# Kernel optimization log

Hardware: AMD Instinct MI355X
Metric: run time of the kernel (lower is better)

## Reference

```python
import jax, jax.numpy as jnp
import numpy as np

N = 50000; E = 800000; B = 500; L = 42
F_IN = 35; HEADS = 10; F_H = 35; F_G = 350
VOCAB = 26; EMB = 128; NF = 16; OUT_DIM = 128; K = 8
NEG_SLOPE = 0.2


def setup_inputs() -> dict:
    key = jax.random.key(0)
    ks = jax.random.split(key, 16)
    inp = {}
    inp['x'] = jax.random.normal(ks[0], (N, F_IN), jnp.float32)
    inp['edge_index'] = jax.random.randint(ks[1], (2, E), 0, N, dtype=jnp.int32)
    inp['batch'] = jnp.sort(jax.random.randint(ks[2], (N,), 0, B, dtype=jnp.int32))
    inp['target'] = jax.random.randint(ks[3], (B, L), 0, VOCAB, dtype=jnp.int32)
    # --- learned parameters ---
    inp['W_gat'] = jax.random.normal(ks[4], (F_IN, HEADS * F_H), jnp.float32) * 0.1
    inp['att_src'] = jax.random.normal(ks[5], (HEADS, F_H), jnp.float32) * 0.1
    inp['att_dst'] = jax.random.normal(ks[6], (HEADS, F_H), jnp.float32) * 0.1
    inp['b_gat'] = jnp.zeros((HEADS * F_H,), jnp.float32)
    inp['W_gcn'] = jax.random.normal(ks[7], (F_G, F_G), jnp.float32) * 0.05
    inp['b_gcn'] = jnp.zeros((F_G,), jnp.float32)
    inp['W_fcg1'] = jax.random.normal(ks[8], (2 * F_G, 1500), jnp.float32) * 0.03
    inp['b_fcg1'] = jnp.zeros((1500,), jnp.float32)
    inp['W_fcg2'] = jax.random.normal(ks[9], (1500, OUT_DIM), jnp.float32) * 0.03
    inp['b_fcg2'] = jnp.zeros((OUT_DIM,), jnp.float32)
    inp['emb_xt'] = jax.random.normal(ks[10], (VOCAB, EMB), jnp.float32) * 0.1
    inp['W_conv'] = jax.random.normal(ks[11], (NF, EMB, K), jnp.float32) * 0.05
    inp['b_conv'] = jnp.zeros((NF,), jnp.float32)
    inp['W_fcxt'] = jax.random.normal(ks[12], (NF * 35, OUT_DIM), jnp.float32) * 0.05
    inp['b_fcxt'] = jnp.zeros((OUT_DIM,), jnp.float32)
    inp['W_fc1'] = jax.random.normal(ks[13], (256, 512), jnp.float32) * 0.05
    inp['b_fc1'] = jnp.zeros((512,), jnp.float32)
    inp['W_out'] = jax.random.normal(ks[14], (512, 1), jnp.float32) * 0.05
    inp['b_out'] = jnp.zeros((1,), jnp.float32)
    return inp


def _add_self_loops(edge_index):
    loop = jnp.arange(N, dtype=edge_index.dtype)
    src = jnp.concatenate([edge_index[0], loop])
    dst = jnp.concatenate([edge_index[1], loop])
    return src, dst


def _gat_conv(x, src, dst, W, att_src, att_dst, b):
    # h: [N, H, C]
    h = (x @ W).reshape(N, HEADS, F_H)
    a_s = jnp.einsum('nhc,hc->nh', h, att_src)  # [N, H]
    a_d = jnp.einsum('nhc,hc->nh', h, att_dst)
    e = jax.nn.leaky_relu(a_s[src] + a_d[dst], NEG_SLOPE)  # [Etot, H]
    # segment softmax over incoming edges per destination node, per head
    m = jax.ops.segment_max(e, dst, num_segments=N)
    m = jnp.where(jnp.isfinite(m), m, 0.0)
    ex = jnp.exp(e - m[dst])
    den = jax.ops.segment_sum(ex, dst, num_segments=N)
    alpha = ex / (den[dst] + 1e-16)  # [Etot, H]
    out = jax.ops.segment_sum(h[src] * alpha[:, :, None], dst, num_segments=N)
    return out.reshape(N, HEADS * F_H) + b, alpha


def _gcn_conv(x, src, dst, W, b):
    deg = jax.ops.segment_sum(jnp.ones_like(dst, jnp.float32), dst, num_segments=N)
    dinv = jnp.where(deg > 0, deg ** -0.5, 0.0)
    norm = dinv[src] * dinv[dst]  # symmetric normalization
    h = x @ W
    return jax.ops.segment_sum(h[src] * norm[:, None], dst, num_segments=N) + b


def reference(x, edge_index, batch, target, W_gat, att_src, att_dst, b_gat,
              W_gcn, b_gcn, W_fcg1, b_fcg1, W_fcg2, b_fcg2, emb_xt,
              W_conv, b_conv, W_fcxt, b_fcxt, W_fc1, b_fc1, W_out, b_out):
    src, dst = _add_self_loops(edge_index)
    # --- graph branch ---
    xg, alpha = _gat_conv(x, src, dst, W_gat, att_src, att_dst, b_gat)
    xg = jax.nn.relu(xg)
    xg = jax.nn.relu(_gcn_conv(xg, src, dst, W_gcn, b_gcn))
    # global max + mean pool per graph
    gmax = jax.ops.segment_max(xg, batch, num_segments=B)
    gsum = jax.ops.segment_sum(xg, batch, num_segments=B)
    cnt = jax.ops.segment_sum(jnp.ones((N,), jnp.float32), batch, num_segments=B)
    gmean = gsum / jnp.maximum(cnt, 1.0)[:, None]
    xg = jnp.concatenate([gmax, gmean], axis=1)  # [B, 700]
    xg = jax.nn.relu(xg @ W_fcg1 + b_fcg1)
    xg = xg @ W_fcg2 + b_fcg2  # [B, 128] (dropout is identity in eval)
    # --- protein branch ---
    emb = emb_xt[target]                      # [B, L, 128]
    emb = jnp.transpose(emb, (0, 2, 1))       # [B, 128, L]
    conv = jax.lax.conv_general_dilated(
        emb, W_conv, window_strides=(1,), padding='VALID',
        dimension_numbers=('NCH', 'OIH', 'NCH'))  # [B, 16, 35]
    conv = conv + b_conv[None, :, None]
    xt = conv.reshape(B, NF * 35)
    xt = xt @ W_fcxt + b_fcxt                 # [B, 128]
    # --- fusion ---
    xc = jnp.concatenate([xg, xt], axis=1)    # [B, 256]
    xc = jax.nn.relu(xc @ W_fc1 + b_fc1)
    out = jax.nn.sigmoid(xc @ W_out + b_out)  # [B, 1]
    return out, alpha
```

## Files before the change

kernel.cpp:

```cpp
#include <hip/hip_runtime.h>
#include <math.h>

#define NN 50000
#define EE 800000
#define BB 500
#define LL 42
#define NHEAD 10
#define FH 35
#define FG 350
#define ETOT (EE + NN)
#define NCHUNK ((NN + 511) / 512)

#define KPAD 384
#define LDH2 512
#define MPAD 50048
#define MB2  512
#define NDW  32

typedef unsigned short ushort_t;
typedef __attribute__((ext_vector_type(8))) short short8v;
typedef __attribute__((ext_vector_type(4))) float float4v;

__device__ __forceinline__ float lrelu(float x) { return x > 0.f ? x : 0.2f * x; }

__device__ __forceinline__ ushort_t f2bf(float f) {
    unsigned int u = __float_as_uint(f);
    u += 0x7fffu + ((u >> 16) & 1u);
    return (ushort_t)(u >> 16);
}
__device__ __forceinline__ float bflo(unsigned u) { return __uint_as_float(u << 16); }
__device__ __forceinline__ float bfhi(unsigned u) { return __uint_as_float(u & 0xffff0000u); }
__device__ __forceinline__ float bfu(ushort_t u) { return __uint_as_float(((unsigned)u) << 16); }
__device__ __forceinline__ unsigned packbf(float a, float b) {
    return (unsigned)f2bf(a) | ((unsigned)f2bf(b) << 16);
}

__device__ __forceinline__ void async_cp16(const void* g, void* l) {
    __builtin_amdgcn_global_load_lds((const __attribute__((address_space(1))) unsigned int*)g,
                                     (__attribute__((address_space(3))) unsigned int*)l, 16, 0, 0);
}

__global__ __launch_bounds__(256) void k_init(int* deg, int* cur) {
    int i = blockIdx.x * 256 + threadIdx.x;
    if (i < NN) { deg[i] = 1; cur[i] = 0; }
}

__global__ __launch_bounds__(256) void k_deg(const int* __restrict__ ei, int* deg) {
    int i = blockIdx.x * 256 + threadIdx.x;
    if (i < EE) atomicAdd(&deg[ei[EE + i]], 1);
}

__global__ __launch_bounds__(512) void k_scan1(const int* __restrict__ deg, int* part) {
    int i = blockIdx.x * 512 + threadIdx.x;
    int lane = threadIdx.x & 63, wv = threadIdx.x >> 6;
    int x = (i < NN) ? deg[i] : 0;
    #pragma unroll
    for (int d = 32; d; d >>= 1) x += __shfl_xor(x, d);
    __shared__ int wsum[8];
    if (lane == 0) wsum[wv] = x;
    __syncthreads();
    if (threadIdx.x == 0) {
        int s = 0;
        #pragma unroll
        for (int w = 0; w < 8; w++) s += wsum[w];
        part[blockIdx.x] = s;
    }
}

__global__ __launch_bounds__(64) void k_scan2(const int* __restrict__ part, int* pscan) {
    int l = threadIdx.x;
    int v0 = (l < NCHUNK) ? part[l] : 0;
    #pragma unroll
    for (int d = 1; d < 64; d <<= 1) { int t = __shfl_up(v0, d); if (l >= d) v0 += t; }
    int tot0 = __shfl(v0, 63);
    int v1 = (64 + l < NCHUNK) ? part[64 + l] : 0;
    #pragma unroll
    for (int d = 1; d < 64; d <<= 1) { int t = __shfl_up(v1, d); if (l >= d) v1 += t; }
    v1 += tot0;
    if (l < NCHUNK) pscan[l] = v0;
    if (64 + l < NCHUNK) pscan[64 + l] = v1;
}

__global__ __launch_bounds__(512) void k_scan3(const int* __restrict__ deg, const int* __restrict__ pscan,
                                               int* offs, float* dinv) {
    int i = blockIdx.x * 512 + threadIdx.x;
    int lane = threadIdx.x & 63, wv = threadIdx.x >> 6;
    int x = (i < NN) ? deg[i] : 0;
    int incl = x;
    #pragma unroll
    for (int d = 1; d < 64; d <<= 1) { int t = __shfl_up(incl, d); if (lane >= d) incl += t; }
    __shared__ int wtot[8];
    if (lane == 63) wtot[wv] = incl;
    __syncthreads();
    int woff = 0;
    for (int w = 0; w < wv; w++) woff += wtot[w];
    int base = (blockIdx.x == 0) ? 0 : pscan[blockIdx.x - 1];
    if (i < NN) {
        offs[i] = base + woff + incl - x;
        dinv[i] = rsqrtf((float)x);
    }
}

__global__ __launch_bounds__(256) void k_scatter(const int* __restrict__ ei, const int* __restrict__ offs,
                                                 int* cur, int* csr_src) {
    int i = blockIdx.x * 256 + threadIdx.x;
    if (i < EE) {
        int s = ei[i], d = ei[EE + i];
        int slot = atomicAdd(&cur[d], 1);
        csr_src[offs[d] + slot] = s;
    } else if (i < ETOT) {
        int v = i - EE;
        int slot = atomicAdd(&cur[v], 1);
        csr_src[offs[v] + slot] = v;
    }
}

__global__ __launch_bounds__(256) void k_prep_att(const float* __restrict__ W_gat, const float* __restrict__ att_s,
                                                  const float* __restrict__ att_d,
                                                  float* __restrict__ wS, float* __restrict__ wD) {
    int i = blockIdx.x * 256 + threadIdx.x;
    if (i >= FG) return;
    int hd = i / 35, c = i % 35;
    float ss = 0.f, dd = 0.f;
    for (int cc = 0; cc < 35; cc++) {
        float w = W_gat[c * FG + hd * 35 + cc];
        ss += w * att_s[hd * 35 + cc];
        dd += w * att_d[hd * 35 + cc];
    }
    wS[i] = ss;
    wD[i] = dd;
}

__global__ __launch_bounds__(256) void k_prep_node(const float* __restrict__ x, const float* __restrict__ wS,
                                                   const float* __restrict__ wD, ushort_t* __restrict__ nd,
                                                   float* __restrict__ a_s, float* __restrict__ a_d) {
    __shared__ float sw[FG], dw[FG];
    int tid = threadIdx.x;
    for (int i = tid; i < FG; i += 256) { sw[i] = wS[i]; dw[i] = wD[i]; }
    __syncthreads();
    int n = blockIdx.x * 256 + tid;
    if (n >= NN) return;
    float xr[35];
    #pragma unroll
    for (int c = 0; c < 35; c++) xr[c] = x[(size_t)n * 35 + c];
    unsigned* xo = (unsigned*)(nd + ((size_t)n << 6));
    #pragma unroll
    for (int w = 0; w < 17; w++) xo[w] = packbf(xr[2 * w], xr[2 * w + 1]);
    xo[17] = packbf(xr[34], 0.f);
    #pragma unroll
    for (int hd = 0; hd < NHEAD; hd++) {
        const float* ws = &sw[hd * 35];
        const float* wd = &dw[hd * 35];
        float as = 0.f, ad = 0.f;
        #pragma unroll
        for (int c = 0; c < 35; c++) { float v = xr[c]; as += v * ws[c]; ad += v * wd[c]; }
        a_s[n * NHEAD + hd] = as;
        a_d[n * NHEAD + hd] = ad;
        xo[18 + hd] = packbf(__expf(as), __expf(0.2f * as));
    }
    xo[28] = 0u; xo[29] = 0u; xo[30] = 0u; xo[31] = 0u;
}

__global__ __launch_bounds__(256) void k_prep_weights(
    const float* __restrict__ Wg, const float* __restrict__ Wc,
    const float* __restrict__ W1, const float* __restrict__ W2,
    const float* __restrict__ WX, const float* __restrict__ WF,
    ushort_t* __restrict__ BD, ushort_t* __restrict__ GC,
    ushort_t* __restrict__ F1, ushort_t* __restrict__ F2,
    ushort_t* __restrict__ FX, ushort_t* __restrict__ FC) {
    int i = blockIdx.x * 256 + threadIdx.x;
    if (i < KPAD * KPAD) {
        int n = i / KPAD, k = i % KPAD;
        int hd = k / 36, cc = k % 36;
        float v = 0.f;
        if (n < FG && cc < 35 && hd == n / 35) v = Wg[cc * FG + n];
        BD[i] = f2bf(v);
        return;
    }
    i -= KPAD * KPAD;
    if (i < KPAD * KPAD) {
        int n = i / KPAD, k = i % KPAD;
        float v = (n < FG && k < FG) ? Wc[k * FG + n] : 0.f;
        GC[i] = f2bf(v);
        return;
    }
    i -= KPAD * KPAD;
    if (i < 704 * 1536) {
        int k = i / 1536, n = i % 1536;
        float v = (k < 700 && n < 1500) ? W1[(size_t)k * 1500 + n] : 0.f;
        F1[(size_t)n * 704 + k] = f2bf(v);
        return;
    }
    i -= 704 * 1536;
    if (i < 1536 * 128) {
        int k = i / 128, n = i % 128;
        float v = (k < 1500) ? W2[(size_t)k * 128 + n] : 0.f;
        F2[(size_t)n * 1536 + k] = f2bf(v);
        return;
    }
    i -= 1536 * 128;
    if (i < 576 * 128) {
        int k = i / 128, n = i % 128;
        float v = (k < 560) ? WX[(size_t)k * 128 + n] : 0.f;
        FX[(size_t)n * 576 + k] = f2bf(v);
        return;
    }
    i -= 576 * 128;
    if (i < 256 * 512) {
        int k = i / 512, n = i % 512;
        FC[(size_t)n * 256 + k] = f2bf(WF[(size_t)k * 512 + n]);
    }
}
#define PREPW_TOTAL (KPAD * KPAD * 2 + 704 * 1536 + 1536 * 128 + 576 * 128 + 256 * 512)

__global__ __launch_bounds__(256) void k_cast_pad(const float* __restrict__ src, ushort_t* __restrict__ dst,
                                                  int M, int K, int MP, int KP) {
    int i = blockIdx.x * 256 + threadIdx.x;
    if (i >= MP * KP) return;
    int r = i / KP, k = i % KP;
    dst[i] = (r < M && k < K) ? f2bf(src[(size_t)r * K + k]) : (ushort_t)0;
}

__global__ __launch_bounds__(256) void k_mfma(const ushort_t* __restrict__ A, const ushort_t* __restrict__ Bt,
                                              void* __restrict__ C, int M, int Nv, int ldc, int lda,
                                              int ksteps, const float* __restrict__ bias, int act, int bf16out,
                                              int bdiag, int nst) {
    __shared__ ushort_t As[128 * 64];
    __shared__ ushort_t Bs[64 * 64];
    int tid = threadIdx.x;
    int wid = tid >> 6, lane = tid & 63;
    int m0 = blockIdx.y * 128, n0 = blockIdx.x * 64;
    int wm0 = (wid >> 1) * 64, wn0 = (wid & 1) * 32;
    int srow = tid >> 3;
    int scol = (tid & 7) * 8;
    float4v acc[4][2] = {{{0.f,0.f,0.f,0.f},{0.f,0.f,0.f,0.f}},
                         {{0.f,0.f,0.f,0.f},{0.f,0.f,0.f,0.f}},
                         {{0.f,0.f,0.f,0.f},{0.f,0.f,0.f,0.f}},
                         {{0.f,0.f,0.f,0.f},{0.f,0.f,0.f,0.f}}};
    int a_off = (wm0 + (lane & 15)) * 64 + (lane >> 4) * 8;
    int b_off = (wn0 + (lane & 15)) * 64 + (lane >> 4) * 8;
    int ks0 = 0, ks1 = ksteps;
    if (bdiag) {
        int hlo = n0 / 35;
        int hhi = (n0 + 63) / 35; if (hhi > 9) hhi = 9;
        ks0 = (hlo * 36) >> 6;
        ks1 = (hhi * 36 + 36 + 63) >> 6;
    }
    for (int ks = ks0; ks < ks1; ks++) {
        int k0 = ks * 64;
        #pragma unroll
        for (int r = 0; r < 4; r++) {
            const ushort_t* g = A + (size_t)(m0 + r * 32 + srow) * lda + k0 + scol;
            async_cp16(g, As + (r * 256 + tid) * 8);
        }
        #pragma unroll
        for (int r = 0; r < 2; r++) {
            const ushort_t* g = Bt + (size_t)(n0 + r * 32 + srow) * lda + k0 + scol;
            async_cp16(g, Bs + (r * 256 + tid) * 8);
        }
        __syncthreads();
        #pragma unroll
        for (int kh = 0; kh < 2; kh++) {
            short8v b0 = *(const short8v*)&Bs[b_off + kh * 32];
            short8v b1 = *(const short8v*)&Bs[b_off + 16 * 64 + kh * 32];
            #pragma unroll
            for (int mi = 0; mi < 4; mi++) {
                short8v a = *(const short8v*)&As[a_off + mi * 16 * 64 + kh * 32];
                acc[mi][0] = __builtin_amdgcn_mfma_f32_16x16x32_bf16(a, b0, acc[mi][0], 0, 0, 0);
                acc[mi][1] = __builtin_amdgcn_mfma_f32_16x16x32_bf16(a, b1, acc[mi][1], 0, 0, 0);
            }
        }
        __syncthreads();
    }
    int lm = m0 + wm0 + (lane >> 4) * 4;
    int lc = n0 + wn0 + (lane & 15);
    #pragma unroll
    for (int mi = 0; mi < 4; mi++) {
        #pragma unroll
        for (int ni = 0; ni < 2; ni++) {
            int col = lc + ni * 16;
            if (col >= nst) continue;
            float bv = (bias != nullptr && col < Nv) ? bias[col] : 0.f;
            #pragma unroll
            for (int r = 0; r < 4; r++) {
                int row = lm + mi * 16 + r;
                if (row >= M) continue;
                float v = acc[mi][ni][r] + bv;
                if (act) v = fmaxf(v, 0.f);
                if (col >= Nv) v = 0.f;
                if (bf16out) ((ushort_t*)C)[(size_t)row * ldc + col] = f2bf(v);
                else         ((float*)C)[(size_t)row * ldc + col] = v;
            }
        }
    }
}

__global__ __launch_bounds__(128) void k_gat_agg(const ushort_t* __restrict__ nd,
                                                 const float* __restrict__ a_d,
                                                 const int* __restrict__ csr_src,
                                                 const int* __restrict__ offs, const int* __restrict__ deg,
                                                 ushort_t* __restrict__ Zb, float* __restrict__ denArr) {
    int wid = blockIdx.x * 2 + (threadIdx.x >> 6);
    int lane = threadIdx.x & 63;
    if (wid >= MPAD) return;
    unsigned* zr = (unsigned*)(Zb + (size_t)wid * KPAD);
    if (wid >= NN) {
        __builtin_nontemporal_store(0u, &zr[lane]);
        __builtin_nontemporal_store(0u, &zr[lane + 64]);
        __builtin_nontemporal_store(0u, &zr[lane + 128]);
        return;
    }
    int o0 = offs[wid], d = deg[wid];
    int h1 = lane / 18,        c1 = lane % 18;
    int h2 = (lane + 64) / 18, c2 = (lane + 64) % 18;
    bool g3 = lane < 52;
    int h3 = g3 ? (lane + 128) / 18 : 7;
    int c3 = g3 ? (lane + 128) % 18 : 0;
    float ad1 = a_d[wid * NHEAD + h1];
    float ad2 = a_d[wid * NHEAD + h2];
    float ad3 = a_d[wid * NHEAD + h3];
    float ev1 = __expf(ad1), ev1b = __expf(0.2f * ad1);
    float ev2 = __expf(ad2), ev2b = __expf(0.2f * ad2);
    float ev3 = __expf(ad3), ev3b = __expf(0.2f * ad3);
    float den1 = 0.f, den2 = 0.f, den3 = 0.f;
    float a1l = 0.f, a1h = 0.f, a2l = 0.f, a2h = 0.f, a3l = 0.f, a3h = 0.f;
    const unsigned* x32 = (const unsigned*)nd;
    int i = 0;
    for (; i + 4 <= d; i += 4) {
        int s[4];
        #pragma unroll
        for (int j = 0; j < 4; j++) s[j] = csr_src[o0 + i + j];
        unsigned p1[4], p2[4], p3[4], u1[4], u2[4], u3[4];
        #pragma unroll
        for (int j = 0; j < 4; j++) {
            const unsigned* r = x32 + ((size_t)s[j] << 5);
            p1[j] = r[18 + h1]; p2[j] = r[18 + h2]; p3[j] = r[18 + h3];
            u1[j] = r[c1]; u2[j] = r[c2]; u3[j] = r[c3];
        }
        #pragma unroll
        for (int j = 0; j < 4; j++) {
            float e1p = bflo(p1[j]) * ev1, e1n = bfhi(p1[j]) * ev1b;
            float e2p = bflo(p2[j]) * ev2, e2n = bfhi(p2[j]) * ev2b;
            float e3p = bflo(p3[j]) * ev3, e3n = bfhi(p3[j]) * ev3b;
            float e1 = (e1p > 1.f) ? e1p : e1n;
            float e2 = (e2p > 1.f) ? e2p : e2n;
            float e3 = (e3p > 1.f) ? e3p : e3n;
            den1 += e1; den2 += e2; den3 += e3;
            a1l += e1 * bflo(u1[j]); a1h += e1 * bfhi(u1[j]);
            a2l += e2 * bflo(u2[j]); a2h += e2 * bfhi(u2[j]);
            a3l += e3 * bflo(u3[j]); a3h += e3 * bfhi(u3[j]);
        }
    }
    for (; i < d; i++) {
        int s = csr_src[o0 + i];
        const unsigned* r = x32 + ((size_t)s << 5);
        unsigned p1v = r[18 + h1], p2v = r[18 + h2], p3v = r[18 + h3];
        unsigned u1v = r[c1], u2v = r[c2], u3v = r[c3];
        float e1p = bflo(p1v) * ev1, e1n = bfhi(p1v) * ev1b;
        float e2p = bflo(p2v) * ev2, e2n = bfhi(p2v) * ev2b;
        float e3p = bflo(p3v) * ev3, e3n = bfhi(p3v) * ev3b;
        float e1 = (e1p > 1.f) ? e1p : e1n;
        float e2 = (e2p > 1.f) ? e2p : e2n;
        float e3 = (e3p > 1.f) ? e3p : e3n;
        den1 += e1; den2 += e2; den3 += e3;
        a1l += e1 * bflo(u1v); a1h += e1 * bfhi(u1v);
        a2l += e2 * bflo(u2v); a2h += e2 * bfhi(u2v);
        a3l += e3 * bflo(u3v); a3h += e3 * bfhi(u3v);
    }
    float* dw = denArr + (size_t)wid * NHEAD;
    if (lane == 0)  { dw[0] = den1; dw[7] = den3; }
    if (lane == 18) dw[1] = den1;
    if (lane == 36) dw[2] = den1;
    if (lane == 54) dw[3] = den1;
    if (lane == 8)  dw[4] = den2;
    if (lane == 26) dw[5] = den2;
    if (lane == 44) dw[6] = den2;
    if (lane == 16) dw[8] = den3;
    if (lane == 34) dw[9] = den3;
    float r1 = 1.f / (den1 + 1e-16f);
    float r2 = 1.f / (den2 + 1e-16f);
    float r3 = 1.f / (den3 + 1e-16f);
    __builtin_nontemporal_store(packbf(a1l * r1, a1h * r1), &zr[lane]);
    __builtin_nontemporal_store(packbf(a2l * r2, a2h * r2), &zr[lane + 64]);
    __builtin_nontemporal_store(g3 ? packbf(a3l * r3, a3h * r3) : 0u, &zr[lane + 128]);
}

__global__ __launch_bounds__(256) void k_alpha(const int* __restrict__ ei, const float* __restrict__ a_s,
                                               const float* __restrict__ a_d, const float* __restrict__ den,
                                               float* __restrict__ alphaOut) {
    int i = blockIdx.x * 256 + threadIdx.x;
    if (i >= ETOT * NHEAD) return;
    int e = i / NHEAD, hd = i % NHEAD;
    int s, dst;
    if (e < EE) { s = ei[e]; dst = ei[EE + e]; }
    else { s = dst = e - EE; }
    float as = a_s[s * NHEAD + hd];
    float ad = a_d[dst * NHEAD + hd];
    float eas  = bfu(f2bf(__expf(as)));
    float eas2 = bfu(f2bf(__expf(0.2f * as)));
    float ep = eas * __expf(ad);
    float en = eas2 * __expf(0.2f * ad);
    float ex = (ep > 1.f) ? ep : en;
    __builtin_nontemporal_store(ex / (den[dst * NHEAD + hd] + 1e-16f), &alphaOut[i]);
}

__global__ __launch_bounds__(128) void k_gcn_agg(const ushort_t* __restrict__ h2b,
                                                 const int* __restrict__ csr_src,
                                                 const int* __restrict__ offs, const int* __restrict__ deg,
                                                 const float* __restrict__ dinv, const float* __restrict__ b_gcn,
                                                 ushort_t* __restrict__ xg2b) {
    int wid = blockIdx.x * 2 + (threadIdx.x >> 6);
    int lane = threadIdx.x & 63;
    if (wid >= NN) return;
    int o0 = offs[wid], d = deg[wid];
    float wv = dinv[wid];
    bool g3 = lane < 48;
    int w3 = g3 ? (lane + 128) : 0;
    float aL0 = 0.f, aH0 = 0.f, aL1 = 0.f, aH1 = 0.f, aL2 = 0.f, aH2 = 0.f;
    const unsigned* h32 = (const unsigned*)h2b;
    int i = 0;
    for (; i + 8 <= d; i += 8) {
        int s[8];
        #pragma unroll
        for (int j = 0; j < 8; j++) s[j] = csr_src[o0 + i + j];
        float q[8]; unsigned ua[8], ub[8], uc[8];
        #pragma unroll
        for (int j = 0; j < 8; j++) {
            q[j] = dinv[s[j]];
            const unsigned* hr = h32 + ((size_t)s[j] << 8);
            ua[j] = hr[lane]; ub[j] = hr[lane + 64]; uc[j] = hr[w3];
        }
        #pragma unroll
        for (int j = 0; j < 8; j++) {
            aL0 += q[j] * bflo(ua[j]); aH0 += q[j] * bfhi(ua[j]);
            aL1 += q[j] * bflo(ub[j]); aH1 += q[j] * bfhi(ub[j]);
            aL2 += q[j] * bflo(uc[j]); aH2 += q[j] * bfhi(uc[j]);
        }
    }
    for (; i < d; i++) {
        int s = csr_src[o0 + i];
        float ws = dinv[s];
        const unsigned* hr = h32 + ((size_t)s << 8);
        unsigned u0 = hr[lane], u1 = hr[lane + 64], u2 = hr[w3];
        aL0 += ws * bflo(u0);  aH0 += ws * bfhi(u0);
        aL1 += ws * bflo(u1);  aH1 += ws * bfhi(u1);
        aL2 += ws * bflo(u2);  aH2 += ws * bfhi(u2);
    }
    unsigned* orow = (unsigned*)(xg2b + (size_t)wid * FG);
    {
        int f = 2 * lane;
        __builtin_nontemporal_store(packbf(fmaxf(wv * aL0 + b_gcn[f], 0.f),
                                           fmaxf(wv * aH0 + b_gcn[f + 1], 0.f)), &orow[lane]);
    }
    {
        int f = 128 + 2 * lane;
        __builtin_nontemporal_store(packbf(fmaxf(wv * aL1 + b_gcn[f], 0.f),
                                           fmaxf(wv * aH1 + b_gcn[f + 1], 0.f)), &orow[64 + lane]);
    }
    if (lane < 47) {
        int f = 256 + 2 * lane;
        __builtin_nontemporal_store(packbf(fmaxf(wv * aL2 + b_gcn[f], 0.f),
                                           fmaxf(wv * aH2 + b_gcn[f + 1], 0.f)), &orow[128 + lane]);
    }
}

__device__ __forceinline__ int lowerB(const int* a, int n, int key) {
    int lo = 0, hi = n;
    while (lo < hi) { int mid = (lo + hi) >> 1; if (a[mid] < key) lo = mid + 1; else hi = mid; }
    return lo;
}

__global__ __launch_bounds__(256) void k_pool(const ushort_t* __restrict__ xg2b, const int* __restrict__ batch,
                                              float* __restrict__ pooled) {
    int g = blockIdx.x;
    int w = threadIdx.x;
    if (w >= 175) return;
    int s = lowerB(batch, NN, g);
    int e = lowerB(batch, NN, g + 1);
    const unsigned* base = (const unsigned*)xg2b;
    float mx0 = -INFINITY, mx1 = -INFINITY, sm0 = 0.f, sm1 = 0.f;
    int n = s;
    for (; n + 2 <= e; n += 2) {
        unsigned ua = base[(size_t)n * 175 + w];
        unsigned ub = base[(size_t)(n + 1) * 175 + w];
        float a0 = bflo(ua), a1 = bfhi(ua), b0 = bflo(ub), b1 = bfhi(ub);
        mx0 = fmaxf(mx0, fmaxf(a0, b0));
        mx1 = fmaxf(mx1, fmaxf(a1, b1));
        sm0 += a0 + b0;
        sm1 += a1 + b1;
    }
    for (; n < e; n++) {
        unsigned ua = base[(size_t)n * 175 + w];
        float a0 = bflo(ua), a1 = bfhi(ua);
        mx0 = fmaxf(mx0, a0);
        mx1 = fmaxf(mx1, a1);
        sm0 += a0;
        sm1 += a1;
    }
    float rc = 1.f / fmaxf((float)(e - s), 1.f);
    pooled[g * 700 + 2 * w]       = mx0;
    pooled[g * 700 + 2 * w + 1]   = mx1;
    pooled[g * 700 + FG + 2 * w]     = sm0 * rc;
    pooled[g * 700 + FG + 2 * w + 1] = sm1 * rc;
}

__global__ __launch_bounds__(256) void k_conv(const int* __restrict__ target, const float* __restrict__ emb,
                                              const float* __restrict__ Wc, const float* __restrict__ bc,
                                              float* __restrict__ xt) {
    __shared__ float embL[26 * 132];
    __shared__ float WL[16 * 8 * 128];
    __shared__ int   tgL[2 * LL];
    int tid = threadIdx.x;
    int b0 = blockIdx.x * 2;
    for (int i = tid; i < 26 * 128; i += 256) {
        int r = i >> 7, e = i & 127;
        embL[r * 132 + e] = emb[i];
    }
    for (int i = tid; i < 16384; i += 256) {
        int f = i >> 10, rem = i & 1023, k = rem >> 7, e = rem & 127;
        WL[i] = Wc[f * 1024 + e * 8 + k];
    }
    if (tid < 2 * LL) tgL[tid] = target[b0 * LL + tid];
    __syncthreads();
    #pragma unroll
    for (int pass = 0; pass < 2; pass++) {
        int r = tid + pass * 256;
        if (r >= 280) break;
        int bl = r / 140, rem = r % 140;
        int fq = rem / 35, t = rem % 35;
        const int* tg = &tgL[bl * LL];
        float ac0 = 0.f, ac1 = 0.f, ac2 = 0.f, ac3 = 0.f;
        for (int k = 0; k < 8; k++) {
            const float* er = &embL[tg[t + k] * 132];
            const float* w0 = &WL[((fq * 4 + 0) * 8 + k) * 128];
            const float* w1 = &WL[((fq * 4 + 1) * 8 + k) * 128];
            const float* w2 = &WL[((fq * 4 + 2) * 8 + k) * 128];
            const float* w3 = &WL[((fq * 4 + 3) * 8 + k) * 128];
            #pragma unroll 8
            for (int e = 0; e < 128; e += 4) {
                float4 a = *(const float4*)&er[e];
                float4 q0 = *(const float4*)&w0[e];
                float4 q1 = *(const float4*)&w1[e];
                float4 q2 = *(const float4*)&w2[e];
                float4 q3 = *(const float4*)&w3[e];
                ac0 += a.x * q0.x + a.y * q0.y + a.z * q0.z + a.w * q0.w;
                ac1 += a.x * q1.x + a.y * q1.y + a.z * q1.z + a.w * q1.w;
                ac2 += a.x * q2.x + a.y * q2.y + a.z * q2.z + a.w * q2.w;
                ac3 += a.x * q3.x + a.y * q3.y + a.z * q3.z + a.w * q3.w;
            }
        }
        int b = b0 + bl, fb = fq * 4;
        xt[b * 560 + (fb + 0) * 35 + t] = ac0 + bc[fb + 0];
        xt[b * 560 + (fb + 1) * 35 + t] = ac1 + bc[fb + 1];
        xt[b * 560 + (fb + 2) * 35 + t] = ac2 + bc[fb + 2];
        xt[b * 560 + (fb + 3) * 35 + t] = ac3 + bc[fb + 3];
    }
}

__global__ __launch_bounds__(256) void k_out(const float* __restrict__ f1, const float* __restrict__ W_out,
                                             const float* __restrict__ b_out, float* __restrict__ out) {
    int wid = (blockIdx.x * blockDim.x + threadIdx.x) >> 6;
    int lane = threadIdx.x & 63;
    if (wid >= BB) return;
    const float* xr = f1 + (size_t)wid * 512;
    float acc = 0.f;
    #pragma unroll
    for (int k = 0; k < 8; k++) acc += xr[lane + k * 64] * W_out[lane + k * 64];
    #pragma unroll
    for (int d = 32; d; d >>= 1) acc += __shfl_xor(acc, d);
    if (lane == 0) out[wid] = 1.f / (1.f + __expf(-(acc + b_out[0])));
}

extern "C" void kernel_launch(void* const* d_in, const int* in_sizes, int n_in,
                              void* d_out, int out_size, void* d_ws, size_t ws_size,
                              hipStream_t stream) {
    const float* x      = (const float*)d_in[0];
    const int*   ei     = (const int*)d_in[1];
    const int*   batch  = (const int*)d_in[2];
    const int*   target = (const int*)d_in[3];
    const float* W_gat  = (const float*)d_in[4];
    const float* att_s  = (const float*)d_in[5];
    const float* att_d  = (const float*)d_in[6];
    const float* b_gat  = (const float*)d_in[7];
    const float* W_gcn  = (const float*)d_in[8];
    const float* b_gcn  = (const float*)d_in[9];
    const float* W_fcg1 = (const float*)d_in[10];
    const float* b_fcg1 = (const float*)d_in[11];
    const float* W_fcg2 = (const float*)d_in[12];
    const float* b_fcg2 = (const float*)d_in[13];
    const float* embxt  = (const float*)d_in[14];
    const float* W_conv = (const float*)d_in[15];
    const float* b_conv = (const float*)d_in[16];
    const float* W_fcxt = (const float*)d_in[17];
    const float* b_fcxt = (const float*)d_in[18];
    const float* W_fc1  = (const float*)d_in[19];
    const float* b_fc1  = (const float*)d_in[20];
    const float* W_out  = (const float*)d_in[21];
    const float* b_out  = (const float*)d_in[22];

    float* out_sig  = (float*)d_out;
    float* alphaOut = (float*)d_out + BB;

    size_t o = 0;
    auto alloc = [&](size_t bytes) -> void* {
        o = (o + 255) & ~(size_t)255;
        void* p = (char*)d_ws + o;
        o += bytes;
        return p;
    };
    int*   deg     = (int*)alloc((size_t)NN * 4);
    int*   cur     = (int*)alloc((size_t)NN * 4);
    int*   offs    = (int*)alloc((size_t)NN * 4);
    int*   part    = (int*)alloc(128 * 4);
    int*   pscan   = (int*)alloc(128 * 4);
    int*   csr_src = (int*)alloc((size_t)ETOT * 4);
    float* dinv    = (float*)alloc((size_t)NN * 4);
    float* a_s     = (float*)alloc((size_t)NN * NHEAD * 4);
    float* a_d     = (float*)alloc((size_t)NN * NHEAD * 4);
    float* denArr  = (float*)alloc((size_t)NN * NHEAD * 4);
    ushort_t* nd   = (ushort_t*)alloc((size_t)NN * 64 * 2);
    float* wS      = (float*)alloc((size_t)FG * 4);
    float* wD      = (float*)alloc((size_t)FG * 4);
    ushort_t* WtBD = (ushort_t*)alloc((size_t)KPAD * KPAD * 2);
    ushort_t* WtGC = (ushort_t*)alloc((size_t)KPAD * KPAD * 2);
    ushort_t* WtF1 = (ushort_t*)alloc((size_t)1536 * 704 * 2);
    ushort_t* WtF2 = (ushort_t*)alloc((size_t)128 * 1536 * 2);
    ushort_t* WtFX = (ushort_t*)alloc((size_t)128 * 576 * 2);
    ushort_t* WtFC = (ushort_t*)alloc((size_t)512 * 256 * 2);
    float* pooled  = (float*)alloc((size_t)BB * 700 * 4);
    ushort_t* pooledb = (ushort_t*)alloc((size_t)MB2 * 704 * 2);
    ushort_t* t1b  = (ushort_t*)alloc((size_t)MB2 * 1536 * 2);
    float* xt      = (float*)alloc((size_t)BB * 560 * 4);
    ushort_t* xtb  = (ushort_t*)alloc((size_t)MB2 * 576 * 2);
    ushort_t* xcb  = (ushort_t*)alloc((size_t)MB2 * 256 * 2);
    float* f1      = (float*)alloc((size_t)MB2 * 512 * 4);
    ushort_t* hb   = (ushort_t*)alloc((size_t)MPAD * LDH2 * 2);
    char*  R2      = (char*)alloc((size_t)NN * FG * 4);
    ushort_t* xg1b = (ushort_t*)R2;
    ushort_t* xg2b = (ushort_t*)R2;
    (void)ws_size; (void)n_in; (void)in_sizes; (void)out_size;

    auto mfma = [&](const ushort_t* A, const ushort_t* Bt, void* C, const float* bias,
                    int M2, int Nv, int NP, int ldc, int KP, int act, int bf16out, int bdiag, int nst) {
        dim3 g(NP / 64, M2 / 128);
        k_mfma<<<g, 256, 0, stream>>>(A, Bt, C, M2, Nv, ldc, KP, KP / 64, bias, act, bf16out, bdiag, nst);
    };

    k_init<<<(NN + 255) / 256, 256, 0, stream>>>(deg, cur);
    k_deg<<<(EE + 255) / 256, 256, 0, stream>>>(ei, deg);
    k_scan1<<<NCHUNK, 512, 0, stream>>>(deg, part);
    k_scan2<<<1, 64, 0, stream>>>(part, pscan);
    k_scan3<<<NCHUNK, 512, 0, stream>>>(deg, pscan, offs, dinv);
    k_scatter<<<(ETOT + 255) / 256, 256, 0, stream>>>(ei, offs, cur, csr_src);

    k_prep_att<<<2, 256, 0, stream>>>(W_gat, att_s, att_d, wS, wD);
    k_prep_node<<<(NN + 255) / 256, 256, 0, stream>>>(x, wS, wD, nd, a_s, a_d);
    k_prep_weights<<<(PREPW_TOTAL + 255) / 256, 256, 0, stream>>>(W_gat, W_gcn, W_fcg1, W_fcg2,
                                                                  W_fcxt, W_fc1,
                                                                  WtBD, WtGC, WtF1, WtF2, WtFX, WtFC);

    k_gat_agg<<<MPAD / 2, 128, 0, stream>>>(nd, a_d, csr_src, offs, deg, hb, denArr);
    k_alpha<<<(ETOT * NHEAD + 255) / 256, 256, 0, stream>>>(ei, a_s, a_d, denArr, alphaOut);
    mfma(hb, WtBD, xg1b, b_gat, MPAD, FG, KPAD, KPAD, KPAD, 1, 1, 1, KPAD);

    mfma(xg1b, WtGC, hb, nullptr, MPAD, FG, KPAD, LDH2, KPAD, 0, 1, 0, 352);
    k_gcn_agg<<<(NN + 1) / 2, 128, 0, stream>>>(hb, csr_src, offs, deg, dinv, b_gcn, xg2b);

    k_pool<<<BB, 256, 0, stream>>>(xg2b, batch, pooled);
    k_cast_pad<<<(MB2 * 704 + 255) / 256, 256, 0, stream>>>(pooled, pooledb, BB, 700, MB2, 704);
    mfma(pooledb, WtF1, t1b, b_fcg1, MB2, 1500, 1536, 1536, 704, 1, 1, 0, 1536);
    mfma(t1b, WtF2, xcb, b_fcg2, MB2, 128, 128, 256, 1536, 0, 1, 0, 128);
    k_conv<<<250, 256, 0, stream>>>(target, embxt, W_conv, b_conv, xt);
    k_cast_pad<<<(MB2 * 576 + 255) / 256, 256, 0, stream>>>(xt, xtb, BB, 560, MB2, 576);
    mfma(xtb, WtFX, xcb + 128, b_fcxt, MB2, 128, 128, 256, 576, 0, 1, 0, 128);
    mfma(xcb, WtFC, f1, b_fc1, MB2, 512, 512, 512, 256, 1, 0, 0, 512);
    k_out<<<(BB + 3) / 4, 256, 0, stream>>>(f1, W_out, b_out, out_sig);
}
```

Baseline: 580.0 us.

## Sort nodes by degree for aggregation, compact GCN row stride, reuse packed exps

Adds a degree histogram, a scan and a permutation scatter so the GAT and GCN aggregation kernels visit destination nodes in descending-degree order, which balances wavefront work and reduces tail imbalance. The GCN intermediate row stride drops from 512 to 352 bf16, shrinking the gathered footprint and improving cache use. k_alpha now reads the precomputed bf16 exp pair from the node buffer instead of recomputing exps from a stored a_s array, so a_s is removed. The cost is three small extra kernel launches and less locality, since sorted order scatters output row writes.

```diff
diff --git a/kernel.cpp b/kernel.cpp
--- a/kernel.cpp
+++ b/kernel.cpp
@@ -12,7 +12,7 @@
 #define NCHUNK ((NN + 511) / 512)
 
 #define KPAD 384
-#define LDH2 512
+#define LDH2 352
 #define MPAD 50048
 #define MB2  512
 #define NDW  32
@@ -40,9 +40,10 @@
                                      (__attribute__((address_space(3))) unsigned int*)l, 16, 0, 0);
 }
 
-__global__ __launch_bounds__(256) void k_init(int* deg, int* cur) {
+__global__ __launch_bounds__(256) void k_init(int* deg, int* cur, int* hist) {
     int i = blockIdx.x * 256 + threadIdx.x;
     if (i < NN) { deg[i] = 1; cur[i] = 0; }
+    if (i < 64) hist[i] = 0;
 }
 
 __global__ __launch_bounds__(256) void k_deg(const int* __restrict__ ei, int* deg) {
@@ -115,6 +116,31 @@
     }
 }
 
+__global__ __launch_bounds__(256) void k_hist(const int* __restrict__ deg, int* hist) {
+    int i = blockIdx.x * 256 + threadIdx.x;
+    if (i >= NN) return;
+    int d = deg[i]; if (d > 63) d = 63;
+    atomicAdd(&hist[63 - d], 1);
+}
+
+__global__ __launch_bounds__(64) void k_hscan(const int* __restrict__ hist, int* cursor) {
+    int l = threadIdx.x;
+    int v = hist[l];
+    int incl = v;
+    #pragma unroll
+    for (int d = 1; d < 64; d <<= 1) { int t = __shfl_up(incl, d); if (l >= d) incl += t; }
+    cursor[l] = incl - v;
+}
+
+__global__ __launch_bounds__(256) void k_pscatter(const int* __restrict__ deg, int* cursor,
+                                                  int* __restrict__ perm) {
+    int i = blockIdx.x * 256 + threadIdx.x;
+    if (i >= NN) return;
+    int d = deg[i]; if (d > 63) d = 63;
+    int slot = atomicAdd(&cursor[63 - d], 1);
+    perm[slot] = i;
+}
+
 __global__ __launch_bounds__(256) void k_prep_att(const float* __restrict__ W_gat, const float* __restrict__ att_s,
                                                   const float* __restrict__ att_d,
                                                   float* __restrict__ wS, float* __restrict__ wD) {
@@ -133,7 +159,7 @@
 
 __global__ __launch_bounds__(256) void k_prep_node(const float* __restrict__ x, const float* __restrict__ wS,
                                                    const float* __restrict__ wD, ushort_t* __restrict__ nd,
-                                                   float* __restrict__ a_s, float* __restrict__ a_d) {
+                                                   float* __restrict__ a_d) {
     __shared__ float sw[FG], dw[FG];
     int tid = threadIdx.x;
     for (int i = tid; i < FG; i += 256) { sw[i] = wS[i]; dw[i] = wD[i]; }
@@ -154,7 +180,6 @@
         float as = 0.f, ad = 0.f;
         #pragma unroll
         for (int c = 0; c < 35; c++) { float v = xr[c]; as += v * ws[c]; ad += v * wd[c]; }
-        a_s[n * NHEAD + hd] = as;
         a_d[n * NHEAD + hd] = ad;
         xo[18 + hd] = packbf(__expf(as), __expf(0.2f * as));
     }
@@ -299,17 +324,20 @@
                                                  const float* __restrict__ a_d,
                                                  const int* __restrict__ csr_src,
                                                  const int* __restrict__ offs, const int* __restrict__ deg,
+                                                 const int* __restrict__ perm,
                                                  ushort_t* __restrict__ Zb, float* __restrict__ denArr) {
-    int wid = blockIdx.x * 2 + (threadIdx.x >> 6);
+    int slot = blockIdx.x * 2 + (threadIdx.x >> 6);
     int lane = threadIdx.x & 63;
-    if (wid >= MPAD) return;
+    if (slot >= MPAD) return;
+    if (slot >= NN) {
+        unsigned* zp = (unsigned*)(Zb + (size_t)slot * KPAD);
+        __builtin_nontemporal_store(0u, &zp[lane]);
+        __builtin_nontemporal_store(0u, &zp[lane + 64]);
+        __builtin_nontemporal_store(0u, &zp[lane + 128]);
+        return;
+    }
+    int wid = perm[slot];
     unsigned* zr = (unsigned*)(Zb + (size_t)wid * KPAD);
-    if (wid >= NN) {
-        __builtin_nontemporal_store(0u, &zr[lane]);
-        __builtin_nontemporal_store(0u, &zr[lane + 64]);
-        __builtin_nontemporal_store(0u, &zr[lane + 128]);
-        return;
-    }
     int o0 = offs[wid], d = deg[wid];
     int h1 = lane / 18,        c1 = lane % 18;
     int h2 = (lane + 64) / 18, c2 = (lane + 64) % 18;
@@ -385,7 +413,7 @@
     __builtin_nontemporal_store(g3 ? packbf(a3l * r3, a3h * r3) : 0u, &zr[lane + 128]);
 }
 
-__global__ __launch_bounds__(256) void k_alpha(const int* __restrict__ ei, const float* __restrict__ a_s,
+__global__ __launch_bounds__(256) void k_alpha(const int* __restrict__ ei, const ushort_t* __restrict__ nd,
                                                const float* __restrict__ a_d, const float* __restrict__ den,
                                                float* __restrict__ alphaOut) {
     int i = blockIdx.x * 256 + threadIdx.x;
@@ -394,12 +422,10 @@
     int s, dst;
     if (e < EE) { s = ei[e]; dst = ei[EE + e]; }
     else { s = dst = e - EE; }
-    float as = a_s[s * NHEAD + hd];
+    unsigned epw = ((const unsigned*)nd)[((size_t)s << 5) + 18 + hd];
     float ad = a_d[dst * NHEAD + hd];
-    float eas  = bfu(f2bf(__expf(as)));
-    float eas2 = bfu(f2bf(__expf(0.2f * as)));
-    float ep = eas * __expf(ad);
-    float en = eas2 * __expf(0.2f * ad);
+    float ep = bflo(epw) * __expf(ad);
+    float en = bfhi(epw) * __expf(0.2f * ad);
     float ex = (ep > 1.f) ? ep : en;
     __builtin_nontemporal_store(ex / (den[dst * NHEAD + hd] + 1e-16f), &alphaOut[i]);
 }
@@ -408,10 +434,12 @@
                                                  const int* __restrict__ csr_src,
                                                  const int* __restrict__ offs, const int* __restrict__ deg,
                                                  const float* __restrict__ dinv, const float* __restrict__ b_gcn,
+                                                 const int* __restrict__ perm,
                                                  ushort_t* __restrict__ xg2b) {
-    int wid = blockIdx.x * 2 + (threadIdx.x >> 6);
+    int slot = blockIdx.x * 2 + (threadIdx.x >> 6);
     int lane = threadIdx.x & 63;
-    if (wid >= NN) return;
+    if (slot >= NN) return;
+    int wid = perm[slot];
     int o0 = offs[wid], d = deg[wid];
     float wv = dinv[wid];
     bool g3 = lane < 48;
@@ -427,7 +455,7 @@
         #pragma unroll
         for (int j = 0; j < 8; j++) {
             q[j] = dinv[s[j]];
-            const unsigned* hr = h32 + ((size_t)s[j] << 8);
+            const unsigned* hr = h32 + (size_t)s[j] * (LDH2 / 2);
             ua[j] = hr[lane]; ub[j] = hr[lane + 64]; uc[j] = hr[w3];
         }
         #pragma unroll
@@ -440,7 +468,7 @@
     for (; i < d; i++) {
         int s = csr_src[o0 + i];
         float ws = dinv[s];
-        const unsigned* hr = h32 + ((size_t)s << 8);
+        const unsigned* hr = h32 + (size_t)s * (LDH2 / 2);
         unsigned u0 = hr[lane], u1 = hr[lane + 64], u2 = hr[w3];
         aL0 += ws * bflo(u0);  aH0 += ws * bfhi(u0);
         aL1 += ws * bflo(u1);  aH1 += ws * bfhi(u1);
@@ -613,9 +641,11 @@
     int*   offs    = (int*)alloc((size_t)NN * 4);
     int*   part    = (int*)alloc(128 * 4);
     int*   pscan   = (int*)alloc(128 * 4);
+    int*   hist    = (int*)alloc(64 * 4);
+    int*   cursor  = (int*)alloc(64 * 4);
+    int*   perm    = (int*)alloc((size_t)NN * 4);
     int*   csr_src = (int*)alloc((size_t)ETOT * 4);
     float* dinv    = (float*)alloc((size_t)NN * 4);
-    float* a_s     = (float*)alloc((size_t)NN * NHEAD * 4);
     float* a_d     = (float*)alloc((size_t)NN * NHEAD * 4);
     float* denArr  = (float*)alloc((size_t)NN * NHEAD * 4);
     ushort_t* nd   = (ushort_t*)alloc((size_t)NN * 64 * 2);
@@ -634,7 +664,7 @@
     ushort_t* xtb  = (ushort_t*)alloc((size_t)MB2 * 576 * 2);
     ushort_t* xcb  = (ushort_t*)alloc((size_t)MB2 * 256 * 2);
     float* f1      = (float*)alloc((size_t)MB2 * 512 * 4);
-    ushort_t* hb   = (ushort_t*)alloc((size_t)MPAD * LDH2 * 2);
+    ushort_t* hb   = (ushort_t*)alloc((size_t)MPAD * KPAD * 2);
     char*  R2      = (char*)alloc((size_t)NN * FG * 4);
     ushort_t* xg1b = (ushort_t*)R2;
     ushort_t* xg2b = (ushort_t*)R2;
@@ -646,25 +676,29 @@
         k_mfma<<<g, 256, 0, stream>>>(A, Bt, C, M2, Nv, ldc, KP, KP / 64, bias, act, bf16out, bdiag, nst);
     };
 
-    k_init<<<(NN + 255) / 256, 256, 0, stream>>>(deg, cur);
+    k_init<<<(NN + 255) / 256, 256, 0, stream>>>(deg, cur, hist);
     k_deg<<<(EE + 255) / 256, 256, 0, stream>>>(ei, deg);
     k_scan1<<<NCHUNK, 512, 0, stream>>>(deg, part);
     k_scan2<<<1, 64, 0, stream>>>(part, pscan);
     k_scan3<<<NCHUNK, 512, 0, stream>>>(deg, pscan, offs, dinv);
     k_scatter<<<(ETOT + 255) / 256, 256, 0, stream>>>(ei, offs, cur, csr_src);
 
+    k_hist<<<(NN + 255) / 256, 256, 0, stream>>>(deg, hist);
+    k_hscan<<<1, 64, 0, stream>>>(hist, cursor);
+    k_pscatter<<<(NN + 255) / 256, 256, 0, stream>>>(deg, cursor, perm);
+
     k_prep_att<<<2, 256, 0, stream>>>(W_gat, att_s, att_d, wS, wD);
-    k_prep_node<<<(NN + 255) / 256, 256, 0, stream>>>(x, wS, wD, nd, a_s, a_d);
+    k_prep_node<<<(NN + 255) / 256, 256, 0, stream>>>(x, wS, wD, nd, a_d);
     k_prep_weights<<<(PREPW_TOTAL + 255) / 256, 256, 0, stream>>>(W_gat, W_gcn, W_fcg1, W_fcg2,
                                                                   W_fcxt, W_fc1,
                                                                   WtBD, WtGC, WtF1, WtF2, WtFX, WtFC);
 
-    k_gat_agg<<<MPAD / 2, 128, 0, stream>>>(nd, a_d, csr_src, offs, deg, hb, denArr);
-    k_alpha<<<(ETOT * NHEAD + 255) / 256, 256, 0, stream>>>(ei, a_s, a_d, denArr, alphaOut);
+    k_gat_agg<<<MPAD / 2, 128, 0, stream>>>(nd, a_d, csr_src, offs, deg, perm, hb, denArr);
+    k_alpha<<<(ETOT * NHEAD + 255) / 256, 256, 0, stream>>>(ei, nd, a_d, denArr, alphaOut);
     mfma(hb, WtBD, xg1b, b_gat, MPAD, FG, KPAD, KPAD, KPAD, 1, 1, 1, KPAD);
 
-    mfma(xg1b, WtGC, hb, nullptr, MPAD, FG, KPAD, LDH2, KPAD, 0, 1, 0, 352);
-    k_gcn_agg<<<(NN + 1) / 2, 128, 0, stream>>>(hb, csr_src, offs, deg, dinv, b_gcn, xg2b);
+    mfma(xg1b, WtGC, hb, nullptr, MPAD, FG, KPAD, LDH2, KPAD, 0, 1, 0, LDH2);
+    k_gcn_agg<<<(NN + 1) / 2, 128, 0, stream>>>(hb, csr_src, offs, deg, dinv, b_gcn, perm, xg2b);
 
     k_pool<<<BB, 256, 0, stream>>>(xg2b, batch, pooled);
     k_cast_pad<<<(MB2 * 704 + 255) / 256, 256, 0, stream>>>(pooled, pooledb, BB, 700, MB2, 704);
```

After: 858.0 us. 47.9% more time.
